# Optimization experiments

Measured on AMD Instinct MI355X. Metric: run time of the kernel, lower is better.

## Reference

```python
import jax, jax.numpy as jnp
import numpy as np

NUM_AGENTS = 64
FEAT_DIM = 524288  # per-agent hidden/state width


def setup_inputs() -> dict:
    key = jax.random.key(0)
    k_h, k_c, k_H, k_C = jax.random.split(key, 4)
    h = jax.random.normal(k_h, (NUM_AGENTS, FEAT_DIM), dtype=jnp.float32)
    c = jax.random.normal(k_c, (NUM_AGENTS, FEAT_DIM), dtype=jnp.float32)
    # learned parameters (torch.randn init in the original module)
    H = jax.random.normal(k_H, (NUM_AGENTS, NUM_AGENTS), dtype=jnp.float32)
    C = jax.random.normal(k_C, (NUM_AGENTS, NUM_AGENTS), dtype=jnp.float32)
    return {"h": h, "c": c, "H": H, "C": C}


def reference(h, c, H, C):
    # hidden = tanh(H @ h + C @ c), shapes: [N,N]@[N,D] -> [N,D]
    hidden = jnp.tanh(jnp.matmul(H, h) + jnp.matmul(C, c))
    # Faithful to source: order[i] stacks hidden[i] (N-1) times and divides
    # by (N-1), so comm[i] == hidden[i] exactly.
    comm = hidden
    return (hidden, comm)
```

## Files before the change

kernel.cpp:

```cpp
#include <hip/hip_runtime.h>

#define NA 64
#define FD 524288
#define FD2 (FD / 2)

__global__ __launch_bounds__(256, 1) void linlayer_kernel(
    const float* __restrict__ h, const float* __restrict__ c,
    const float* __restrict__ Hm, const float* __restrict__ Cm,
    float* __restrict__ out)
{
    const int tid = blockIdx.x * blockDim.x + threadIdx.x;

    const float2* __restrict__ h2 = (const float2*)h;
    const float2* __restrict__ c2 = (const float2*)c;
    float2* __restrict__ o2 = (float2*)out;

#pragma unroll 1
    for (int col = 0; col < 2; ++col) {
        const int d2 = tid + col * (FD2 / 2);

        float2 acc[NA];
#pragma unroll
        for (int i = 0; i < NA; ++i) { acc[i].x = 0.f; acc[i].y = 0.f; }

        float2 hv = h2[d2];
        float2 cv = c2[d2];

#pragma unroll 1
        for (int j = 0; j < NA; ++j) {
            const int jn = (j + 1) & (NA - 1);
            const float2 hn = h2[(size_t)jn * FD2 + d2];
            const float2 cn = c2[(size_t)jn * FD2 + d2];
#pragma unroll
            for (int i = 0; i < NA; ++i) {
                const float Hij = Hm[i * NA + j];
                const float Cij = Cm[i * NA + j];
                acc[i].x = fmaf(Hij, hv.x, fmaf(Cij, cv.x, acc[i].x));
                acc[i].y = fmaf(Hij, hv.y, fmaf(Cij, cv.y, acc[i].y));
            }
            hv = hn; cv = cn;
        }

#pragma unroll
        for (int i = 0; i < NA; ++i) {
            float2 t;
            {
                const float e = __expf(2.0f * acc[i].x);
                t.x = 1.0f - 2.0f / (e + 1.0f);
            }
            {
                const float e = __expf(2.0f * acc[i].y);
                t.y = 1.0f - 2.0f / (e + 1.0f);
            }
            o2[(size_t)i * FD2 + d2] = t;
            o2[(size_t)(NA + i) * FD2 + d2] = t;
        }
    }
}

extern "C" void kernel_launch(void* const* d_in, const int* in_sizes, int n_in,
                              void* d_out, int out_size, void* d_ws, size_t ws_size,
                              hipStream_t stream) {
    const float* h  = (const float*)d_in[0];
    const float* c  = (const float*)d_in[1];
    const float* Hm = (const float*)d_in[2];
    const float* Cm = (const float*)d_in[3];
    float* out = (float*)d_out;

    dim3 block(256);
    dim3 grid((FD2 / 2) / 256);
    hipLaunchKernelGGL(linlayer_kernel, grid, block, 0, stream,
                       h, c, Hm, Cm, out);
}
```

Baseline: 523.1 us.

## Use scalar-per-thread columns with j-tiled loads, higher occupancy, nontemporal stores

Each thread now computes one feature column (scalar accumulators) instead of two float2 columns in sequence. The grid grows to one thread per column, and launch bounds allow up to 4 blocks per CU. The j loop is tiled by 8, so eight h and c rows are loaded up front before the FMAs, giving more memory-level parallelism. Output stores become nontemporal to avoid polluting the cache. The cost is 64 accumulators plus 16 loaded values per thread, which may still strain the register budget at the higher occupancy target, and the coalesced accesses shrink from 8-byte to 4-byte.

```diff
diff --git a/kernel.cpp b/kernel.cpp
--- a/kernel.cpp
+++ b/kernel.cpp
@@ -2,59 +2,50 @@
 
 #define NA 64
 #define FD 524288
-#define FD2 (FD / 2)
+#define JT 8
 
-__global__ __launch_bounds__(256, 1) void linlayer_kernel(
+__global__ __launch_bounds__(256, 4) void linlayer_kernel(
     const float* __restrict__ h, const float* __restrict__ c,
     const float* __restrict__ Hm, const float* __restrict__ Cm,
     float* __restrict__ out)
 {
-    const int tid = blockIdx.x * blockDim.x + threadIdx.x;
+    const int d = blockIdx.x * blockDim.x + threadIdx.x;
 
-    const float2* __restrict__ h2 = (const float2*)h;
-    const float2* __restrict__ c2 = (const float2*)c;
-    float2* __restrict__ o2 = (float2*)out;
+    const float* __restrict__ hp = h + d;
+    const float* __restrict__ cp = c + d;
+
+    float acc[NA];
+#pragma unroll
+    for (int i = 0; i < NA; ++i) acc[i] = 0.f;
 
 #pragma unroll 1
-    for (int col = 0; col < 2; ++col) {
-        const int d2 = tid + col * (FD2 / 2);
-
-        float2 acc[NA];
+    for (int jt = 0; jt < NA; jt += JT) {
+        float hv[JT], cv[JT];
 #pragma unroll
-        for (int i = 0; i < NA; ++i) { acc[i].x = 0.f; acc[i].y = 0.f; }
-
-        float2 hv = h2[d2];
-        float2 cv = c2[d2];
-
-#pragma unroll 1
-        for (int j = 0; j < NA; ++j) {
-            const int jn = (j + 1) & (NA - 1);
-            const float2 hn = h2[(size_t)jn * FD2 + d2];
-            const float2 cn = c2[(size_t)jn * FD2 + d2];
-#pragma unroll
-            for (int i = 0; i < NA; ++i) {
-                const float Hij = Hm[i * NA + j];
-                const float Cij = Cm[i * NA + j];
-                acc[i].x = fmaf(Hij, hv.x, fmaf(Cij, cv.x, acc[i].x));
-                acc[i].y = fmaf(Hij, hv.y, fmaf(Cij, cv.y, acc[i].y));
-            }
-            hv = hn; cv = cn;
+        for (int jj = 0; jj < JT; ++jj) {
+            hv[jj] = hp[(size_t)(jt + jj) * FD];
+            cv[jj] = cp[(size_t)(jt + jj) * FD];
         }
 
 #pragma unroll
         for (int i = 0; i < NA; ++i) {
-            float2 t;
-            {
-                const float e = __expf(2.0f * acc[i].x);
-                t.x = 1.0f - 2.0f / (e + 1.0f);
+            float a = acc[i];
+#pragma unroll
+            for (int jj = 0; jj < JT; ++jj) {
+                a = fmaf(Hm[i * NA + jt + jj], hv[jj], a);
+                a = fmaf(Cm[i * NA + jt + jj], cv[jj], a);
             }
-            {
-                const float e = __expf(2.0f * acc[i].y);
-                t.y = 1.0f - 2.0f / (e + 1.0f);
-            }
-            o2[(size_t)i * FD2 + d2] = t;
-            o2[(size_t)(NA + i) * FD2 + d2] = t;
+            acc[i] = a;
         }
+    }
+
+    float* __restrict__ op = out + d;
+#pragma unroll
+    for (int i = 0; i < NA; ++i) {
+        const float e = __expf(2.0f * acc[i]);
+        const float t = 1.0f - 2.0f / (e + 1.0f);
+        __builtin_nontemporal_store(t, &op[(size_t)i * FD]);
+        __builtin_nontemporal_store(t, &op[(size_t)(NA + i) * FD]);
     }
 }
 
@@ -68,7 +59,7 @@
     float* out = (float*)d_out;
 
     dim3 block(256);
-    dim3 grid((FD2 / 2) / 256);
+    dim3 grid(FD / 256);
     hipLaunchKernelGGL(linlayer_kernel, grid, block, 0, stream,
                        h, c, Hm, Cm, out);
 }
```

After: 743.7 us. 42.2% more time.

## Split output rows across waves to cut registers and raise occupancy

Applied to the files above, without the earlier changes.

Each block now covers 64 float2 columns, and its four waves each compute 16 of the 64 output rows instead of one thread computing all rows for two columns. This shrinks the accumulator array from 64 to 16 float2, freeing registers so more waves can be resident and memory latency is better hidden. In exchange, each wave rereads the full h and c columns, and relies on cache sharing within the block to avoid a fourfold increase in input traffic.

```diff
diff --git a/kernel.cpp b/kernel.cpp
--- a/kernel.cpp
+++ b/kernel.cpp
@@ -3,58 +3,55 @@
 #define NA 64
 #define FD 524288
 #define FD2 (FD / 2)
+#define ROWS 16
 
-__global__ __launch_bounds__(256, 1) void linlayer_kernel(
+__global__ __launch_bounds__(256) void linlayer_kernel(
     const float* __restrict__ h, const float* __restrict__ c,
     const float* __restrict__ Hm, const float* __restrict__ Cm,
     float* __restrict__ out)
 {
-    const int tid = blockIdx.x * blockDim.x + threadIdx.x;
+    const int lane = threadIdx.x & 63;
+    int i0 = (threadIdx.x >> 6) * ROWS;
+    i0 = __builtin_amdgcn_readfirstlane(i0);
+
+    const int col2 = blockIdx.x * 64 + lane;
 
     const float2* __restrict__ h2 = (const float2*)h;
     const float2* __restrict__ c2 = (const float2*)c;
     float2* __restrict__ o2 = (float2*)out;
 
-#pragma unroll 1
-    for (int col = 0; col < 2; ++col) {
-        const int d2 = tid + col * (FD2 / 2);
+    const float* __restrict__ Hr = Hm + i0 * NA;
+    const float* __restrict__ Cr = Cm + i0 * NA;
 
-        float2 acc[NA];
+    float2 acc[ROWS];
 #pragma unroll
-        for (int i = 0; i < NA; ++i) { acc[i].x = 0.f; acc[i].y = 0.f; }
+    for (int i = 0; i < ROWS; ++i) { acc[i].x = 0.f; acc[i].y = 0.f; }
 
-        float2 hv = h2[d2];
-        float2 cv = c2[d2];
+    float2 hv = h2[col2];
+    float2 cv = c2[col2];
 
 #pragma unroll 1
-        for (int j = 0; j < NA; ++j) {
-            const int jn = (j + 1) & (NA - 1);
-            const float2 hn = h2[(size_t)jn * FD2 + d2];
-            const float2 cn = c2[(size_t)jn * FD2 + d2];
+    for (int j = 0; j < NA; ++j) {
+        const int jn = (j + 1) & (NA - 1);
+        const float2 hn = h2[(size_t)jn * FD2 + col2];
+        const float2 cn = c2[(size_t)jn * FD2 + col2];
 #pragma unroll
-            for (int i = 0; i < NA; ++i) {
-                const float Hij = Hm[i * NA + j];
-                const float Cij = Cm[i * NA + j];
-                acc[i].x = fmaf(Hij, hv.x, fmaf(Cij, cv.x, acc[i].x));
-                acc[i].y = fmaf(Hij, hv.y, fmaf(Cij, cv.y, acc[i].y));
-            }
-            hv = hn; cv = cn;
+        for (int i = 0; i < ROWS; ++i) {
+            const float Hij = Hr[i * NA + j];
+            const float Cij = Cr[i * NA + j];
+            acc[i].x = fmaf(Hij, hv.x, fmaf(Cij, cv.x, acc[i].x));
+            acc[i].y = fmaf(Hij, hv.y, fmaf(Cij, cv.y, acc[i].y));
         }
+        hv = hn; cv = cn;
+    }
 
 #pragma unroll
-        for (int i = 0; i < NA; ++i) {
-            float2 t;
-            {
-                const float e = __expf(2.0f * acc[i].x);
-                t.x = 1.0f - 2.0f / (e + 1.0f);
-            }
-            {
-                const float e = __expf(2.0f * acc[i].y);
-                t.y = 1.0f - 2.0f / (e + 1.0f);
-            }
-            o2[(size_t)i * FD2 + d2] = t;
-            o2[(size_t)(NA + i) * FD2 + d2] = t;
-        }
+    for (int i = 0; i < ROWS; ++i) {
+        float2 t;
+        { const float e = __expf(2.0f * acc[i].x); t.x = 1.0f - 2.0f / (e + 1.0f); }
+        { const float e = __expf(2.0f * acc[i].y); t.y = 1.0f - 2.0f / (e + 1.0f); }
+        o2[(size_t)(i0 + i) * FD2 + col2] = t;
+        o2[(size_t)(NA + i0 + i) * FD2 + col2] = t;
     }
 }
 
@@ -68,7 +65,7 @@
     float* out = (float*)d_out;
 
     dim3 block(256);
-    dim3 grid((FD2 / 2) / 256);
+    dim3 grid(FD2 / 64);
     hipLaunchKernelGGL(linlayer_kernel, grid, block, 0, stream,
                        h, c, Hm, Cm, out);
 }
```

After: 488.8 us. 6.5% less time.
